# Kernel optimization log

Hardware: AMD Instinct MI355X
Metric: run time of the kernel (lower is better)

## Reference

```python
import jax, jax.numpy as jnp
import numpy as np

LN_EPS = 1e-5

def _simple_rmsnorm(x):
    # zeta SimpleRMSNorm: F.normalize(x, dim=-1) * sqrt(d)
    d = x.shape[-1]
    n = jnp.linalg.norm(x, axis=-1, keepdims=True)
    return x / jnp.maximum(n, 1e-12) * jnp.sqrt(jnp.asarray(d, x.dtype))

def _act_quant(x):
    # per-token int8 absmax quant with straight-through estimator
    scale = 127.0 / jnp.clip(jnp.max(jnp.abs(x), axis=-1, keepdims=True), 1e-5)
    y = jnp.clip(jnp.round(x * scale), -128, 127) / scale
    return x + jax.lax.stop_gradient(y - x)

def _weight_quant(w):
    # ternary weight quant (BitNet b1.58) with STE
    scale = 1.0 / jnp.clip(jnp.mean(jnp.abs(w)), 1e-5)
    u = jnp.clip(jnp.round(w * scale), -1, 1) / scale
    return w + jax.lax.stop_gradient(u - w)

def _bitlinear(x, w, b):
    xq = _act_quant(_simple_rmsnorm(x))
    wq = _weight_quant(w)
    return xq @ wq.T + b

def setup_inputs() -> dict:
    key = jax.random.key(0)
    ks = jax.random.split(key, 9)
    B, C, H, W = 16, 64, 128, 128
    inner = 4 * C
    return {
        'x':    jax.random.normal(ks[0], (B, C, H, W), jnp.float32),
        'dw_w': jax.random.normal(ks[1], (C, 1, 3, 3), jnp.float32) * 0.1,
        'dw_b': jax.random.normal(ks[2], (C,), jnp.float32) * 0.02,
        'pw_w': jax.random.normal(ks[3], (C, C), jnp.float32) * (1.0 / np.sqrt(C)),
        'pw_b': jax.random.normal(ks[4], (C,), jnp.float32) * 0.02,
        'ln_w': jnp.ones((C,), jnp.float32),
        'ln_b': jnp.zeros((C,), jnp.float32),
        'w1':   jax.random.normal(ks[5], (inner, C), jnp.float32) * (1.0 / np.sqrt(C)),
        'b1':   jax.random.normal(ks[6], (inner,), jnp.float32) * 0.02,
        'w2':   jax.random.normal(ks[7], (C, inner), jnp.float32) * (1.0 / np.sqrt(inner)),
        'b2':   jax.random.normal(ks[8], (C,), jnp.float32) * 0.02,
    }

def reference(x, dw_w, dw_b, pw_w, pw_b, ln_w, ln_b, w1, b1, w2, b2):
    B, C, H, W = x.shape
    # depthwise 3x3 conv (groups=C), padding=1
    h = jax.lax.conv_general_dilated(
        x, dw_w, window_strides=(1, 1), padding='SAME',
        feature_group_count=C,
        dimension_numbers=('NCHW', 'OIHW', 'NCHW')) + dw_b[None, :, None, None]
    # pointwise 1x1 conv C -> C
    h = jnp.einsum('bchw,oc->bohw', h, pw_w) + pw_b[None, :, None, None]
    # LayerNorm over channels on tokens [B, HW, C]
    t = h.transpose(0, 2, 3, 1).reshape(B, H * W, C)
    mu = jnp.mean(t, axis=-1, keepdims=True)
    var = jnp.var(t, axis=-1, keepdims=True)
    tn = (t - mu) * jax.lax.rsqrt(var + LN_EPS) * ln_w + ln_b
    # BitFeedForward: BitLinear -> GELU -> BitLinear
    f = _bitlinear(tn, w1, b1)
    f = jax.nn.gelu(f, approximate=False)
    f = _bitlinear(f, w2, b2)
    # residual add, back to NCHW
    return h + f.reshape(B, H, W, C).transpose(0, 3, 1, 2)
```

## Files before the change

kernel.cpp:

```cpp
#include <hip/hip_runtime.h>

#define DEVINL __device__ __forceinline__

typedef __attribute__((ext_vector_type(4))) int i32x4;
typedef __attribute__((ext_vector_type(4))) float f32x4;
typedef __attribute__((ext_vector_type(8))) __bf16 bf16x8;

DEVINL float rcp_nr(float x) {
  float r = __builtin_amdgcn_rcpf(x);
  return r * (2.0f - x * r);
}
DEVINL float rsq_nr(float x) {
  float r = __builtin_amdgcn_rsqf(x);
  return r * (1.5f - 0.5f * x * r * r);
}
DEVINL float gelu_f(float x) {
  float z = fabsf(x) * 0.7071067811865476f;
  float t = rcp_nr(fmaf(0.3275911f, z, 1.0f));
  float p = fmaf(1.061405429f, t, -1.453152027f);
  p = fmaf(p, t, 1.421413741f);
  p = fmaf(p, t, -0.284496736f);
  p = fmaf(p, t, 0.254829592f);
  p = p * t;
  float er = fmaf(-p, __expf(-z * z), 1.0f);
  er = copysignf(er, x);
  return 0.5f * x * (1.0f + er);
}

DEVINL unsigned packq4(float a, float b, float c, float d, float scale) {
  int ia = (int)fminf(fmaxf(rintf(a * scale), -1.f), 1.f);
  int ib = (int)fminf(fmaxf(rintf(b * scale), -1.f), 1.f);
  int ic = (int)fminf(fmaxf(rintf(c * scale), -1.f), 1.f);
  int id = (int)fminf(fmaxf(rintf(d * scale), -1.f), 1.f);
  return (unsigned)(ia & 255) | ((unsigned)(ib & 255) << 8) |
         ((unsigned)(ic & 255) << 16) | ((unsigned)(id & 255) << 24);
}

DEVINL unsigned packq8(float a, float b, float c, float d, float s) {
  int q0 = (int)fminf(fmaxf(rintf(a * s), -128.f), 127.f);
  int q1 = (int)fminf(fmaxf(rintf(b * s), -128.f), 127.f);
  int q2 = (int)fminf(fmaxf(rintf(c * s), -128.f), 127.f);
  int q3 = (int)fminf(fmaxf(rintf(d * s), -128.f), 127.f);
  return (unsigned)(q0 & 255) | ((unsigned)(q1 & 255) << 8) |
         ((unsigned)(q2 & 255) << 16) | ((unsigned)(q3 & 255) << 24);
}

DEVINL long long mk64(unsigned lo, unsigned hi) {
  return (long long)(((unsigned long long)hi << 32) | (unsigned long long)lo);
}

__global__ __launch_bounds__(256) void k_prep(
    const float* __restrict__ w1, const float* __restrict__ w2,
    const float* __restrict__ pww, float* __restrict__ scales,
    unsigned* __restrict__ u1f, unsigned* __restrict__ u2f,
    unsigned short* __restrict__ pwbf) {
  const int tid = threadIdx.x;
  const int bx = blockIdx.x;

  if (bx == 2) {
    for (int e = tid; e < 4096; e += 256) {
      int n2 = e >> 10, kh = (e >> 9) & 1, ln = (e >> 3) & 63, j = e & 7;
      int c = ln & 15, hh = ln >> 4;
      float v = pww[(n2 * 16 + c) * 64 + kh * 32 + hh * 8 + j];
      __bf16 hb = (__bf16)v;
      __bf16 lb = (__bf16)(v - (float)hb);
      pwbf[e] = __builtin_bit_cast(unsigned short, hb);
      pwbf[e + 4096] = __builtin_bit_cast(unsigned short, lb);
    }
    return;
  }

  __shared__ double red[4];
  __shared__ float mclip_s;
  const float* w = (bx == 0) ? w1 : w2;

  double s = 0.0;
  for (int e = tid; e < 16384; e += 256) s += (double)fabsf(w[e]);
  #pragma unroll
  for (int m = 32; m; m >>= 1) s += __shfl_xor(s, m, 64);
  if ((tid & 63) == 0) red[tid >> 6] = s;
  __syncthreads();
  if (tid == 0) {
    double tot = red[0] + red[1] + red[2] + red[3];
    float mc = fmaxf((float)(tot / 16384.0), 1e-5f);
    scales[bx] = mc;
    mclip_s = mc;
  }
  __syncthreads();
  const float scale = 1.0f / mclip_s;

  if (bx == 0) {
    for (int e = tid; e < 4096; e += 256) {
      int n = e >> 8, lane = (e >> 2) & 63, word = e & 3;
      int r = n * 16 + (lane & 15);
      int kdw = (word >> 1) * 8 + (lane >> 4) * 2 + (word & 1);
      const float* src = w1 + (r * 16 + kdw) * 4;
      u1f[e] = packq4(src[0], src[1], src[2], src[3], scale);
    }
  } else {
    for (int e = tid; e < 4096; e += 256) {
      int ks = e >> 9, n2 = (e >> 7) & 3, lane = (e >> 1) & 63, word = e & 1;
      int r = n2 * 16 + (lane & 15);
      int kdw = ks * 8 + (lane >> 4) * 2 + word;
      const float* src = w2 + (r * 64 + kdw) * 4;
      u2f[e] = packq4(src[0], src[1], src[2], src[3], scale);
    }
  }
}

__global__ __launch_bounds__(256, 8) void k_dw(
    const float* __restrict__ x, const float* __restrict__ dww,
    const float* __restrict__ dwb, unsigned* __restrict__ hout) {
  const int tid = threadIdx.x;
  const int px = tid & 127, yq = tid >> 7;
  const int y0 = (blockIdx.x * 2 + yq) * 4;
  const int c = blockIdx.y, bz = blockIdx.z;
  const float* xc = x + (((size_t)bz * 64 + c) << 14);

  float wv[9];
  #pragma unroll
  for (int i = 0; i < 9; ++i) wv[i] = dww[c * 9 + i];
  const float bias = dwb[c];

  float v[6][3];
  #pragma unroll
  for (int ry = 0; ry < 6; ++ry) {
    int iy = y0 - 1 + ry;
    bool yok = (unsigned)iy < 128u;
    const float* row = xc + ((size_t)(iy & 127) << 7);
    #pragma unroll
    for (int dx = 0; dx < 3; ++dx) {
      int ix = px - 1 + dx;
      v[ry][dx] = (yok && (unsigned)ix < 128u) ? row[ix & 127] : 0.f;
    }
  }

  unsigned* op = hout + (((size_t)bz * 64 + c) << 14) + ((size_t)y0 << 7) + px;
  #pragma unroll
  for (int oy = 0; oy < 4; ++oy) {
    float acc = bias;
    #pragma unroll
    for (int ky = 0; ky < 3; ++ky)
      #pragma unroll
      for (int kx = 0; kx < 3; ++kx)
        acc = fmaf(v[oy + ky][kx], wv[ky * 3 + kx], acc);
    __bf16 hb = (__bf16)acc;
    __bf16 lb = (__bf16)(acc - (float)hb);
    op[(size_t)oy << 7] =
        ((unsigned)__builtin_bit_cast(unsigned short, hb) << 16) |
        (unsigned)__builtin_bit_cast(unsigned short, lb);
  }
}

__global__ __launch_bounds__(256, 4) void k_fused(
    const float* __restrict__ pwb, const float* __restrict__ lnw,
    const float* __restrict__ lnb, const float* __restrict__ b1,
    const float* __restrict__ b2, const float* __restrict__ scales,
    const unsigned* __restrict__ u1f, const unsigned* __restrict__ u2f,
    const uint4* __restrict__ pwf, const unsigned* hpk, float* dout) {
  __shared__ __align__(16) unsigned wq[16 * 18];
  __shared__ __align__(16) unsigned qf2[16 * 70];
  __shared__ float redA[2][4][16], redB[2][4][16];

  const int tid = threadIdx.x;
  const int w = tid >> 6, lane = tid & 63;
  const int col = lane & 15, hi = lane >> 4;
  const int y = blockIdx.x, bz = blockIdx.y;
  const size_t gbase = ((size_t)bz * 64) << 14;

  const int chb = w * 16 + 4 * hi;
  float pwbr[4], lnw_r[4], lnb_r[4], b2r[4];
  #pragma unroll
  for (int r = 0; r < 4; ++r) {
    pwbr[r] = pwb[chb + r];
    lnw_r[r] = lnw[chb + r];
    lnb_r[r] = lnb[chb + r];
    b2r[r] = b2[chb + r];
  }
  const float sc0 = scales[0], m2c = scales[1];

  uint4 pwa[2], pwl[2];
  #pragma unroll
  for (int kh = 0; kh < 2; ++kh) {
    pwa[kh] = pwf[(w * 2 + kh) * 64 + lane];
    pwl[kh] = pwf[(w * 2 + kh) * 64 + lane + 512];
  }
  uint4 w1r[4];
  #pragma unroll
  for (int n = 0; n < 4; ++n)
    w1r[n] = *(const uint4*)&u1f[(((w * 4 + n) * 64) + lane) * 4];
  uint2 w2r[8];
  #pragma unroll
  for (int ks = 0; ks < 8; ++ks)
    w2r[ks] = *(const uint2*)&u2f[(((ks * 4 + w) * 64) + lane) * 2];

  #pragma unroll 1
  for (int it = 0; it < 8; ++it) {
    const int gcol = y * 128 + it * 16 + col;

    bf16x8 bh[2], bl[2];
    #pragma unroll
    for (int kh = 0; kh < 2; ++kh) {
      unsigned u[8];
      #pragma unroll
      for (int j = 0; j < 8; ++j)
        u[j] = hpk[gbase + (((size_t)(kh * 32 + hi * 8 + j)) << 14) + gcol];
      uint4 bhw, blw;
      #pragma unroll
      for (int jw = 0; jw < 4; ++jw) {
        ((unsigned*)&bhw)[jw] =
            __builtin_amdgcn_perm(u[2 * jw + 1], u[2 * jw], 0x07060302u);
        ((unsigned*)&blw)[jw] =
            __builtin_amdgcn_perm(u[2 * jw + 1], u[2 * jw], 0x05040100u);
      }
      bh[kh] = __builtin_bit_cast(bf16x8, bhw);
      bl[kh] = __builtin_bit_cast(bf16x8, blw);
    }

    f32x4 pacc = {0.f, 0.f, 0.f, 0.f};
    #pragma unroll
    for (int kh = 0; kh < 2; ++kh) {
      bf16x8 ah = __builtin_bit_cast(bf16x8, pwa[kh]);
      bf16x8 al = __builtin_bit_cast(bf16x8, pwl[kh]);
      pacc = __builtin_amdgcn_mfma_f32_16x16x32_bf16(ah, bh[kh], pacc, 0, 0, 0);
      pacc = __builtin_amdgcn_mfma_f32_16x16x32_bf16(ah, bl[kh], pacc, 0, 0, 0);
      pacc = __builtin_amdgcn_mfma_f32_16x16x32_bf16(al, bh[kh], pacc, 0, 0, 0);
    }
    float hacc[4];
    #pragma unroll
    for (int r = 0; r < 4; ++r) hacc[r] = pacc[r] + pwbr[r];

    float s1 = 0.f, q1 = 0.f;
    #pragma unroll
    for (int r = 0; r < 4; ++r) {
      s1 += hacc[r];
      q1 = fmaf(hacc[r], hacc[r], q1);
    }
    s1 += __shfl_xor(s1, 16, 64); s1 += __shfl_xor(s1, 32, 64);
    q1 += __shfl_xor(q1, 16, 64); q1 += __shfl_xor(q1, 32, 64);
    if (hi == 0) { redA[0][w][col] = s1; redB[0][w][col] = q1; }
    __syncthreads();
    float S = redA[0][0][col] + redA[0][1][col] + redA[0][2][col] + redA[0][3][col];
    float Q = redB[0][0][col] + redB[0][1][col] + redB[0][2][col] + redB[0][3][col];
    const float mu = S * (1.f / 64.f);
    const float var = fmaxf(Q * (1.f / 64.f) - mu * mu, 0.f);
    const float istd = rsq_nr(var + 1e-5f);

    float tn[4];
    float s2 = 0.f, am = 0.f;
    #pragma unroll
    for (int r = 0; r < 4; ++r) {
      float t = (hacc[r] - mu) * istd * lnw_r[r] + lnb_r[r];
      tn[r] = t;
      s2 = fmaf(t, t, s2);
      am = fmaxf(am, fabsf(t));
    }
    s2 += __shfl_xor(s2, 16, 64); s2 += __shfl_xor(s2, 32, 64);
    am = fmaxf(am, __shfl_xor(am, 16, 64));
    am = fmaxf(am, __shfl_xor(am, 32, 64));
    if (hi == 0) { redA[1][w][col] = s2; redB[1][w][col] = am; }
    __syncthreads();
    float S2 = redA[1][0][col] + redA[1][1][col] + redA[1][2][col] + redA[1][3][col];
    float AM = fmaxf(fmaxf(redB[1][0][col], redB[1][1][col]),
                     fmaxf(redB[1][2][col], redB[1][3][col]));

    const float n1 = sqrtf(S2);
    const float inv1 = rcp_nr(fmaxf(n1, 1e-12f));
    const float axc1 = fmaxf(AM * 8.f * inv1, 1e-5f);
    const float sx1 = 127.f * rcp_nr(axc1);
    const float qs1 = 8.f * inv1 * sx1;
    const float fsc1 = sc0 * axc1 * (1.f / 127.f);

    wq[col * 18 + w * 4 + hi] = packq8(tn[0], tn[1], tn[2], tn[3], qs1);
    __syncthreads();

    const uint2 bw0 = *(const uint2*)&wq[col * 18 + 2 * hi];
    const uint2 bw1 = *(const uint2*)&wq[col * 18 + 8 + 2 * hi];
    const long long bq0 = mk64(bw0.x, bw0.y);
    const long long bq1 = mk64(bw1.x, bw1.y);

    float g[4][4];
    float sum2 = 0.f, am2 = 0.f;
    #pragma unroll
    for (int n = 0; n < 4; ++n) {
      i32x4 cc = {0, 0, 0, 0};
      cc = __builtin_amdgcn_mfma_i32_16x16x32_i8(mk64(w1r[n].x, w1r[n].y), bq0,
                                                 cc, 0, 0, 0);
      cc = __builtin_amdgcn_mfma_i32_16x16x32_i8(mk64(w1r[n].z, w1r[n].w), bq1,
                                                 cc, 0, 0, 0);
      const float4 bb = *(const float4*)&b1[w * 64 + n * 16 + 4 * hi];
      #pragma unroll
      for (int r = 0; r < 4; ++r) {
        float f = (float)cc[r] * fsc1 + ((const float*)&bb)[r];
        float gg = gelu_f(f);
        g[n][r] = gg;
        sum2 = fmaf(gg, gg, sum2);
        am2 = fmaxf(am2, fabsf(gg));
      }
    }
    sum2 += __shfl_xor(sum2, 16, 64); sum2 += __shfl_xor(sum2, 32, 64);
    am2 = fmaxf(am2, __shfl_xor(am2, 16, 64));
    am2 = fmaxf(am2, __shfl_xor(am2, 32, 64));
    if (hi == 0) { redA[0][w][col] = sum2; redB[0][w][col] = am2; }
    __syncthreads();
    float S4 = redA[0][0][col] + redA[0][1][col] + redA[0][2][col] + redA[0][3][col];
    float AM2 = fmaxf(fmaxf(redB[0][0][col], redB[0][1][col]),
                      fmaxf(redB[0][2][col], redB[0][3][col]));

    const float n2v = sqrtf(S4);
    const float inv2 = rcp_nr(fmaxf(n2v, 1e-12f));
    const float axc2 = fmaxf(AM2 * 16.f * inv2, 1e-5f);
    const float sx2 = 127.f * rcp_nr(axc2);
    const float qs2 = 16.f * inv2 * sx2;
    const float fsc2 = m2c * axc2 * (1.f / 127.f);

    #pragma unroll
    for (int n = 0; n < 4; ++n)
      qf2[col * 70 + w * 16 + n * 4 + hi] =
          packq8(g[n][0], g[n][1], g[n][2], g[n][3], qs2);
    __syncthreads();

    i32x4 c2 = {0, 0, 0, 0};
    #pragma unroll
    for (int ks = 0; ks < 8; ++ks) {
      const uint2 bw = *(const uint2*)&qf2[col * 70 + ks * 8 + 2 * hi];
      const long long bfr = mk64(bw.x, bw.y);
      const long long afr = mk64(w2r[ks].x, w2r[ks].y);
      c2 = __builtin_amdgcn_mfma_i32_16x16x32_i8(afr, bfr, c2, 0, 0, 0);
    }

    #pragma unroll
    for (int r = 0; r < 4; ++r) {
      float v = (float)c2[r] * fsc2 + b2r[r] + hacc[r];
      dout[gbase + (((size_t)(chb + r)) << 14) + gcol] = v;
    }
  }
}

extern "C" void kernel_launch(void* const* d_in, const int* in_sizes, int n_in,
                              void* d_out, int out_size, void* d_ws, size_t ws_size,
                              hipStream_t stream) {
  (void)in_sizes; (void)n_in; (void)out_size; (void)ws_size;
  const float* x   = (const float*)d_in[0];
  const float* dww = (const float*)d_in[1];
  const float* dwb = (const float*)d_in[2];
  const float* pww = (const float*)d_in[3];
  const float* pwb = (const float*)d_in[4];
  const float* lnw = (const float*)d_in[5];
  const float* lnb = (const float*)d_in[6];
  const float* w1  = (const float*)d_in[7];
  const float* b1  = (const float*)d_in[8];
  const float* w2  = (const float*)d_in[9];
  const float* b2  = (const float*)d_in[10];
  float* out = (float*)d_out;

  float* scales = (float*)d_ws;
  unsigned* u1f = (unsigned*)((char*)d_ws + 16);
  unsigned* u2f = u1f + 4096;
  unsigned short* pwbf = (unsigned short*)((char*)d_ws + 16 + 32768);

  hipLaunchKernelGGL(k_prep, dim3(3), dim3(256), 0, stream,
                     w1, w2, pww, scales, u1f, u2f, pwbf);
  hipLaunchKernelGGL(k_dw, dim3(16, 64, 16), dim3(256), 0, stream,
                     x, dww, dwb, (unsigned*)out);
  hipLaunchKernelGGL(k_fused, dim3(128, 16), dim3(256), 0, stream,
                     pwb, lnw, lnb, b1, b2, scales, u1f, u2f,
                     (const uint4*)pwbf, (const unsigned*)out, out);
}
```

Before: 130.2 us.

## Process two 16-pixel tiles per iteration and trim GELU/quant instruction counts

The fused kernel loop now handles 32 pixels per iteration as two 16-column subtiles, halving the number of block barriers per pixel and interleaving independent MFMA chains for ILP. GELU is rewritten with raw rcp/exp2 and an algebraically folded erf, the Newton-refined rcp/rsq are dropped, packq8 uses med3 clamps plus byte perms, and b1 is hoisted into registers. Launch bounds drop from 4 to 3 waves occupancy to give more registers, at the cost of occupancy and slightly lower precision in reciprocals.

```diff
diff --git a/kernel.cpp b/kernel.cpp
--- a/kernel.cpp
+++ b/kernel.cpp
@@ -6,25 +6,19 @@
 typedef __attribute__((ext_vector_type(4))) float f32x4;
 typedef __attribute__((ext_vector_type(8))) __bf16 bf16x8;
 
-DEVINL float rcp_nr(float x) {
-  float r = __builtin_amdgcn_rcpf(x);
-  return r * (2.0f - x * r);
-}
-DEVINL float rsq_nr(float x) {
-  float r = __builtin_amdgcn_rsqf(x);
-  return r * (1.5f - 0.5f * x * r * r);
-}
 DEVINL float gelu_f(float x) {
-  float z = fabsf(x) * 0.7071067811865476f;
-  float t = rcp_nr(fmaf(0.3275911f, z, 1.0f));
+  float ax = fabsf(x);
+  float z = ax * 0.7071067811865476f;
+  float t = __builtin_amdgcn_rcpf(fmaf(0.3275911f, z, 1.0f));
   float p = fmaf(1.061405429f, t, -1.453152027f);
   p = fmaf(p, t, 1.421413741f);
   p = fmaf(p, t, -0.284496736f);
   p = fmaf(p, t, 0.254829592f);
   p = p * t;
-  float er = fmaf(-p, __expf(-z * z), 1.0f);
-  er = copysignf(er, x);
-  return 0.5f * x * (1.0f + er);
+  float e = __builtin_amdgcn_exp2f(x * x * -0.7213475204444817f);
+  float b = 0.5f * ax;
+  float s = fmaf(0.5f, x, b);
+  return fmaf(-(b * p), e, s);
 }
 
 DEVINL unsigned packq4(float a, float b, float c, float d, float scale) {
@@ -37,12 +31,13 @@
 }
 
 DEVINL unsigned packq8(float a, float b, float c, float d, float s) {
-  int q0 = (int)fminf(fmaxf(rintf(a * s), -128.f), 127.f);
-  int q1 = (int)fminf(fmaxf(rintf(b * s), -128.f), 127.f);
-  int q2 = (int)fminf(fmaxf(rintf(c * s), -128.f), 127.f);
-  int q3 = (int)fminf(fmaxf(rintf(d * s), -128.f), 127.f);
-  return (unsigned)(q0 & 255) | ((unsigned)(q1 & 255) << 8) |
-         ((unsigned)(q2 & 255) << 16) | ((unsigned)(q3 & 255) << 24);
+  unsigned q0 = (unsigned)(int)__builtin_amdgcn_fmed3f(rintf(a * s), -128.f, 127.f);
+  unsigned q1 = (unsigned)(int)__builtin_amdgcn_fmed3f(rintf(b * s), -128.f, 127.f);
+  unsigned q2 = (unsigned)(int)__builtin_amdgcn_fmed3f(rintf(c * s), -128.f, 127.f);
+  unsigned q3 = (unsigned)(int)__builtin_amdgcn_fmed3f(rintf(d * s), -128.f, 127.f);
+  unsigned t0 = __builtin_amdgcn_perm(q1, q0, 0x00000400u);
+  unsigned t1 = __builtin_amdgcn_perm(q3, q2, 0x00000400u);
+  return __builtin_amdgcn_perm(t1, t0, 0x05040100u);
 }
 
 DEVINL long long mk64(unsigned lo, unsigned hi) {
@@ -152,23 +147,23 @@
   }
 }
 
-__global__ __launch_bounds__(256, 4) void k_fused(
+__global__ __launch_bounds__(256, 3) void k_fused(
     const float* __restrict__ pwb, const float* __restrict__ lnw,
     const float* __restrict__ lnb, const float* __restrict__ b1,
     const float* __restrict__ b2, const float* __restrict__ scales,
     const unsigned* __restrict__ u1f, const unsigned* __restrict__ u2f,
     const uint4* __restrict__ pwf, const unsigned* hpk, float* dout) {
-  __shared__ __align__(16) unsigned wq[16 * 18];
-  __shared__ __align__(16) unsigned qf2[16 * 70];
-  __shared__ float redA[2][4][16], redB[2][4][16];
+  __shared__ __align__(16) unsigned wq[32 * 18];
+  __shared__ __align__(16) unsigned qf2[32 * 70];
+  __shared__ float redA[2][4][32], redB[2][4][32];
 
   const int tid = threadIdx.x;
   const int w = tid >> 6, lane = tid & 63;
   const int col = lane & 15, hi = lane >> 4;
   const int y = blockIdx.x, bz = blockIdx.y;
   const size_t gbase = ((size_t)bz * 64) << 14;
-
   const int chb = w * 16 + 4 * hi;
+
   float pwbr[4], lnw_r[4], lnb_r[4], b2r[4];
   #pragma unroll
   for (int r = 0; r < 4; ++r) {
@@ -177,6 +172,10 @@
     lnb_r[r] = lnb[chb + r];
     b2r[r] = b2[chb + r];
   }
+  float4 b1r[4];
+  #pragma unroll
+  for (int n = 0; n < 4; ++n)
+    b1r[n] = *(const float4*)&b1[w * 64 + n * 16 + 4 * hi];
   const float sc0 = scales[0], m2c = scales[1];
 
   uint4 pwa[2], pwl[2];
@@ -195,145 +194,194 @@
     w2r[ks] = *(const uint2*)&u2f[(((ks * 4 + w) * 64) + lane) * 2];
 
   #pragma unroll 1
-  for (int it = 0; it < 8; ++it) {
-    const int gcol = y * 128 + it * 16 + col;
-
-    bf16x8 bh[2], bl[2];
-    #pragma unroll
-    for (int kh = 0; kh < 2; ++kh) {
-      unsigned u[8];
-      #pragma unroll
-      for (int j = 0; j < 8; ++j)
-        u[j] = hpk[gbase + (((size_t)(kh * 32 + hi * 8 + j)) << 14) + gcol];
-      uint4 bhw, blw;
-      #pragma unroll
-      for (int jw = 0; jw < 4; ++jw) {
-        ((unsigned*)&bhw)[jw] =
-            __builtin_amdgcn_perm(u[2 * jw + 1], u[2 * jw], 0x07060302u);
-        ((unsigned*)&blw)[jw] =
-            __builtin_amdgcn_perm(u[2 * jw + 1], u[2 * jw], 0x05040100u);
-      }
-      bh[kh] = __builtin_bit_cast(bf16x8, bhw);
-      bl[kh] = __builtin_bit_cast(bf16x8, blw);
-    }
-
-    f32x4 pacc = {0.f, 0.f, 0.f, 0.f};
-    #pragma unroll
-    for (int kh = 0; kh < 2; ++kh) {
-      bf16x8 ah = __builtin_bit_cast(bf16x8, pwa[kh]);
-      bf16x8 al = __builtin_bit_cast(bf16x8, pwl[kh]);
-      pacc = __builtin_amdgcn_mfma_f32_16x16x32_bf16(ah, bh[kh], pacc, 0, 0, 0);
-      pacc = __builtin_amdgcn_mfma_f32_16x16x32_bf16(ah, bl[kh], pacc, 0, 0, 0);
-      pacc = __builtin_amdgcn_mfma_f32_16x16x32_bf16(al, bh[kh], pacc, 0, 0, 0);
-    }
-    float hacc[4];
-    #pragma unroll
-    for (int r = 0; r < 4; ++r) hacc[r] = pacc[r] + pwbr[r];
-
-    float s1 = 0.f, q1 = 0.f;
-    #pragma unroll
-    for (int r = 0; r < 4; ++r) {
-      s1 += hacc[r];
-      q1 = fmaf(hacc[r], hacc[r], q1);
-    }
-    s1 += __shfl_xor(s1, 16, 64); s1 += __shfl_xor(s1, 32, 64);
-    q1 += __shfl_xor(q1, 16, 64); q1 += __shfl_xor(q1, 32, 64);
-    if (hi == 0) { redA[0][w][col] = s1; redB[0][w][col] = q1; }
+  for (int it = 0; it < 4; ++it) {
+    const int gc = y * 128 + it * 32 + col;
+
+    float hacc[2][4];
+    #pragma unroll
+    for (int t2 = 0; t2 < 2; ++t2) {
+      bf16x8 bh[2], bl[2];
+      #pragma unroll
+      for (int kh = 0; kh < 2; ++kh) {
+        unsigned u[8];
+        #pragma unroll
+        for (int j = 0; j < 8; ++j)
+          u[j] = hpk[gbase + (((size_t)(kh * 32 + hi * 8 + j)) << 14) + gc +
+                     16 * t2];
+        uint4 bhw, blw;
+        #pragma unroll
+        for (int jw = 0; jw < 4; ++jw) {
+          ((unsigned*)&bhw)[jw] =
+              __builtin_amdgcn_perm(u[2 * jw + 1], u[2 * jw], 0x07060302u);
+          ((unsigned*)&blw)[jw] =
+              __builtin_amdgcn_perm(u[2 * jw + 1], u[2 * jw], 0x05040100u);
+        }
+        bh[kh] = __builtin_bit_cast(bf16x8, bhw);
+        bl[kh] = __builtin_bit_cast(bf16x8, blw);
+      }
+      f32x4 pacc = {0.f, 0.f, 0.f, 0.f};
+      #pragma unroll
+      for (int kh = 0; kh < 2; ++kh) {
+        bf16x8 ah = __builtin_bit_cast(bf16x8, pwa[kh]);
+        bf16x8 al = __builtin_bit_cast(bf16x8, pwl[kh]);
+        pacc = __builtin_amdgcn_mfma_f32_16x16x32_bf16(ah, bh[kh], pacc, 0, 0, 0);
+        pacc = __builtin_amdgcn_mfma_f32_16x16x32_bf16(ah, bl[kh], pacc, 0, 0, 0);
+        pacc = __builtin_amdgcn_mfma_f32_16x16x32_bf16(al, bh[kh], pacc, 0, 0, 0);
+      }
+      #pragma unroll
+      for (int r = 0; r < 4; ++r) hacc[t2][r] = pacc[r] + pwbr[r];
+    }
+
+    #pragma unroll
+    for (int t2 = 0; t2 < 2; ++t2) {
+      float s1 = 0.f, q1 = 0.f;
+      #pragma unroll
+      for (int r = 0; r < 4; ++r) {
+        s1 += hacc[t2][r];
+        q1 = fmaf(hacc[t2][r], hacc[t2][r], q1);
+      }
+      s1 += __shfl_xor(s1, 16, 64); s1 += __shfl_xor(s1, 32, 64);
+      q1 += __shfl_xor(q1, 16, 64); q1 += __shfl_xor(q1, 32, 64);
+      if (hi == 0) {
+        redA[0][w][col + 16 * t2] = s1;
+        redB[0][w][col + 16 * t2] = q1;
+      }
+    }
     __syncthreads();
-    float S = redA[0][0][col] + redA[0][1][col] + redA[0][2][col] + redA[0][3][col];
-    float Q = redB[0][0][col] + redB[0][1][col] + redB[0][2][col] + redB[0][3][col];
-    const float mu = S * (1.f / 64.f);
-    const float var = fmaxf(Q * (1.f / 64.f) - mu * mu, 0.f);
-    const float istd = rsq_nr(var + 1e-5f);
-
-    float tn[4];
-    float s2 = 0.f, am = 0.f;
-    #pragma unroll
-    for (int r = 0; r < 4; ++r) {
-      float t = (hacc[r] - mu) * istd * lnw_r[r] + lnb_r[r];
-      tn[r] = t;
-      s2 = fmaf(t, t, s2);
-      am = fmaxf(am, fabsf(t));
-    }
-    s2 += __shfl_xor(s2, 16, 64); s2 += __shfl_xor(s2, 32, 64);
-    am = fmaxf(am, __shfl_xor(am, 16, 64));
-    am = fmaxf(am, __shfl_xor(am, 32, 64));
-    if (hi == 0) { redA[1][w][col] = s2; redB[1][w][col] = am; }
+    float mu[2], istd[2];
+    #pragma unroll
+    for (int t2 = 0; t2 < 2; ++t2) {
+      int ct = col + 16 * t2;
+      float S = redA[0][0][ct] + redA[0][1][ct] + redA[0][2][ct] + redA[0][3][ct];
+      float Q = redB[0][0][ct] + redB[0][1][ct] + redB[0][2][ct] + redB[0][3][ct];
+      mu[t2] = S * (1.f / 64.f);
+      float var = fmaxf(Q * (1.f / 64.f) - mu[t2] * mu[t2], 0.f);
+      istd[t2] = __builtin_amdgcn_rsqf(var + 1e-5f);
+    }
+
+    float tn[2][4];
+    #pragma unroll
+    for (int t2 = 0; t2 < 2; ++t2) {
+      float s2 = 0.f, am = 0.f;
+      #pragma unroll
+      for (int r = 0; r < 4; ++r) {
+        float t = (hacc[t2][r] - mu[t2]) * istd[t2] * lnw_r[r] + lnb_r[r];
+        tn[t2][r] = t;
+        s2 = fmaf(t, t, s2);
+        am = fmaxf(am, fabsf(t));
+      }
+      s2 += __shfl_xor(s2, 16, 64); s2 += __shfl_xor(s2, 32, 64);
+      am = fmaxf(am, __shfl_xor(am, 16, 64));
+      am = fmaxf(am, __shfl_xor(am, 32, 64));
+      if (hi == 0) {
+        redA[1][w][col + 16 * t2] = s2;
+        redB[1][w][col + 16 * t2] = am;
+      }
+    }
     __syncthreads();
-    float S2 = redA[1][0][col] + redA[1][1][col] + redA[1][2][col] + redA[1][3][col];
-    float AM = fmaxf(fmaxf(redB[1][0][col], redB[1][1][col]),
-                     fmaxf(redB[1][2][col], redB[1][3][col]));
-
-    const float n1 = sqrtf(S2);
-    const float inv1 = rcp_nr(fmaxf(n1, 1e-12f));
-    const float axc1 = fmaxf(AM * 8.f * inv1, 1e-5f);
-    const float sx1 = 127.f * rcp_nr(axc1);
-    const float qs1 = 8.f * inv1 * sx1;
-    const float fsc1 = sc0 * axc1 * (1.f / 127.f);
-
-    wq[col * 18 + w * 4 + hi] = packq8(tn[0], tn[1], tn[2], tn[3], qs1);
+    float qs1[2], fsc1[2];
+    #pragma unroll
+    for (int t2 = 0; t2 < 2; ++t2) {
+      int ct = col + 16 * t2;
+      float S2 = redA[1][0][ct] + redA[1][1][ct] + redA[1][2][ct] + redA[1][3][ct];
+      float AM = fmaxf(fmaxf(redB[1][0][ct], redB[1][1][ct]),
+                       fmaxf(redB[1][2][ct], redB[1][3][ct]));
+      float n1 = sqrtf(S2);
+      float inv1 = __builtin_amdgcn_rcpf(fmaxf(n1, 1e-12f));
+      float axc1 = fmaxf(AM * 8.f * inv1, 1e-5f);
+      float sx1 = 127.f * __builtin_amdgcn_rcpf(axc1);
+      qs1[t2] = 8.f * inv1 * sx1;
+      fsc1[t2] = sc0 * axc1 * (1.f / 127.f);
+    }
+
+    #pragma unroll
+    for (int t2 = 0; t2 < 2; ++t2)
+      wq[(col + 16 * t2) * 18 + w * 4 + hi] =
+          packq8(tn[t2][0], tn[t2][1], tn[t2][2], tn[t2][3], qs1[t2]);
     __syncthreads();
 
-    const uint2 bw0 = *(const uint2*)&wq[col * 18 + 2 * hi];
-    const uint2 bw1 = *(const uint2*)&wq[col * 18 + 8 + 2 * hi];
-    const long long bq0 = mk64(bw0.x, bw0.y);
-    const long long bq1 = mk64(bw1.x, bw1.y);
-
-    float g[4][4];
-    float sum2 = 0.f, am2 = 0.f;
+    long long bq0[2], bq1[2];
+    #pragma unroll
+    for (int t2 = 0; t2 < 2; ++t2) {
+      const unsigned* row = &wq[(col + 16 * t2) * 18];
+      bq0[t2] = mk64(row[2 * hi], row[2 * hi + 1]);
+      bq1[t2] = mk64(row[8 + 2 * hi], row[8 + 2 * hi + 1]);
+    }
+    float g[2][4][4];
+    float sum2[2] = {0.f, 0.f}, am2[2] = {0.f, 0.f};
     #pragma unroll
     for (int n = 0; n < 4; ++n) {
-      i32x4 cc = {0, 0, 0, 0};
-      cc = __builtin_amdgcn_mfma_i32_16x16x32_i8(mk64(w1r[n].x, w1r[n].y), bq0,
-                                                 cc, 0, 0, 0);
-      cc = __builtin_amdgcn_mfma_i32_16x16x32_i8(mk64(w1r[n].z, w1r[n].w), bq1,
-                                                 cc, 0, 0, 0);
-      const float4 bb = *(const float4*)&b1[w * 64 + n * 16 + 4 * hi];
+      const long long a0 = mk64(w1r[n].x, w1r[n].y);
+      const long long a1 = mk64(w1r[n].z, w1r[n].w);
+      #pragma unroll
+      for (int t2 = 0; t2 < 2; ++t2) {
+        i32x4 cc = {0, 0, 0, 0};
+        cc = __builtin_amdgcn_mfma_i32_16x16x32_i8(a0, bq0[t2], cc, 0, 0, 0);
+        cc = __builtin_amdgcn_mfma_i32_16x16x32_i8(a1, bq1[t2], cc, 0, 0, 0);
+        #pragma unroll
+        for (int r = 0; r < 4; ++r) {
+          float f = (float)cc[r] * fsc1[t2] + ((const float*)&b1r[n])[r];
+          float gg = gelu_f(f);
+          g[t2][n][r] = gg;
+          sum2[t2] = fmaf(gg, gg, sum2[t2]);
+          am2[t2] = fmaxf(am2[t2], fabsf(gg));
+        }
+      }
+    }
+    #pragma unroll
+    for (int t2 = 0; t2 < 2; ++t2) {
+      sum2[t2] += __shfl_xor(sum2[t2], 16, 64);
+      sum2[t2] += __shfl_xor(sum2[t2], 32, 64);
+      am2[t2] = fmaxf(am2[t2], __shfl_xor(am2[t2], 16, 64));
+      am2[t2] = fmaxf(am2[t2], __shfl_xor(am2[t2], 32, 64));
+      if (hi == 0) {
+        redA[0][w][col + 16 * t2] = sum2[t2];
+        redB[0][w][col + 16 * t2] = am2[t2];
+      }
+    }
+    __syncthreads();
+    float qs2[2], fsc2[2];
+    #pragma unroll
+    for (int t2 = 0; t2 < 2; ++t2) {
+      int ct = col + 16 * t2;
+      float S4 = redA[0][0][ct] + redA[0][1][ct] + redA[0][2][ct] + redA[0][3][ct];
+      float AM2 = fmaxf(fmaxf(redB[0][0][ct], redB[0][1][ct]),
+                        fmaxf(redB[0][2][ct], redB[0][3][ct]));
+      float n2v = sqrtf(S4);
+      float inv2 = __builtin_amdgcn_rcpf(fmaxf(n2v, 1e-12f));
+      float axc2 = fmaxf(AM2 * 16.f * inv2, 1e-5f);
+      float sx2 = 127.f * __builtin_amdgcn_rcpf(axc2);
+      qs2[t2] = 16.f * inv2 * sx2;
+      fsc2[t2] = m2c * axc2 * (1.f / 127.f);
+    }
+
+    #pragma unroll
+    for (int t2 = 0; t2 < 2; ++t2)
+      #pragma unroll
+      for (int n = 0; n < 4; ++n)
+        qf2[(col + 16 * t2) * 70 + w * 16 + n * 4 + hi] = packq8(
+            g[t2][n][0], g[t2][n][1], g[t2][n][2], g[t2][n][3], qs2[t2]);
+    __syncthreads();
+
+    i32x4 c2[2] = {{0, 0, 0, 0}, {0, 0, 0, 0}};
+    #pragma unroll
+    for (int ks = 0; ks < 8; ++ks) {
+      const long long afr = mk64(w2r[ks].x, w2r[ks].y);
+      #pragma unroll
+      for (int t2 = 0; t2 < 2; ++t2) {
+        const unsigned* brow = &qf2[(col + 16 * t2) * 70 + ks * 8 + 2 * hi];
+        c2[t2] = __builtin_amdgcn_mfma_i32_16x16x32_i8(afr, mk64(brow[0], brow[1]),
+                                                       c2[t2], 0, 0, 0);
+      }
+    }
+
+    #pragma unroll
+    for (int t2 = 0; t2 < 2; ++t2)
       #pragma unroll
       for (int r = 0; r < 4; ++r) {
-        float f = (float)cc[r] * fsc1 + ((const float*)&bb)[r];
-        float gg = gelu_f(f);
-        g[n][r] = gg;
-        sum2 = fmaf(gg, gg, sum2);
-        am2 = fmaxf(am2, fabsf(gg));
-      }
-    }
-    sum2 += __shfl_xor(sum2, 16, 64); sum2 += __shfl_xor(sum2, 32, 64);
-    am2 = fmaxf(am2, __shfl_xor(am2, 16, 64));
-    am2 = fmaxf(am2, __shfl_xor(am2, 32, 64));
-    if (hi == 0) { redA[0][w][col] = sum2; redB[0][w][col] = am2; }
-    __syncthreads();
-    float S4 = redA[0][0][col] + redA[0][1][col] + redA[0][2][col] + redA[0][3][col];
-    float AM2 = fmaxf(fmaxf(redB[0][0][col], redB[0][1][col]),
-                      fmaxf(redB[0][2][col], redB[0][3][col]));
-
-    const float n2v = sqrtf(S4);
-    const float inv2 = rcp_nr(fmaxf(n2v, 1e-12f));
-    const float axc2 = fmaxf(AM2 * 16.f * inv2, 1e-5f);
-    const float sx2 = 127.f * rcp_nr(axc2);
-    const float qs2 = 16.f * inv2 * sx2;
-    const float fsc2 = m2c * axc2 * (1.f / 127.f);
-
-    #pragma unroll
-    for (int n = 0; n < 4; ++n)
-      qf2[col * 70 + w * 16 + n * 4 + hi] =
-          packq8(g[n][0], g[n][1], g[n][2], g[n][3], qs2);
-    __syncthreads();
-
-    i32x4 c2 = {0, 0, 0, 0};
-    #pragma unroll
-    for (int ks = 0; ks < 8; ++ks) {
-      const uint2 bw = *(const uint2*)&qf2[col * 70 + ks * 8 + 2 * hi];
-      const long long bfr = mk64(bw.x, bw.y);
-      const long long afr = mk64(w2r[ks].x, w2r[ks].y);
-      c2 = __builtin_amdgcn_mfma_i32_16x16x32_i8(afr, bfr, c2, 0, 0, 0);
-    }
-
-    #pragma unroll
-    for (int r = 0; r < 4; ++r) {
-      float v = (float)c2[r] * fsc2 + b2r[r] + hacc[r];
-      dout[gbase + (((size_t)(chb + r)) << 14) + gcol] = v;
-    }
+        float v = (float)c2[t2][r] * fsc2[t2] + b2r[r] + hacc[t2][r];
+        dout[gbase + (((size_t)(chb + r)) << 14) + gc + 16 * t2] = v;
+      }
   }
 }
 
```

Result: slower. 138.8 us (+6.6%).
